# Performance work log

Measured on AMD Instinct MI355X. Metric: run time of the kernel, lower is better.

## Reference

```python
import jax, jax.numpy as jnp
import numpy as np

B, C, H, W = 2, 64, 64, 64
C2 = C // 2
N = H * W


def conv1x1(x, w, b):
    # x: (B,Cin,H,W), w: (Cout,Cin), b: (Cout,)
    return jnp.einsum('bchw,oc->bohw', x, w) + b[None, :, None, None]


def setup_inputs() -> dict:
    key = jax.random.key(0)
    ks = jax.random.split(key, 20)
    s = 0.05
    d = {
        'x1': jax.random.normal(ks[0], (B, C, H, W), jnp.float32),
        'x2': jax.random.normal(ks[1], (B, C, H, W), jnp.float32),
        'wq1': jax.random.normal(ks[2], (C2, C), jnp.float32) * s,
        'bq1': jax.random.normal(ks[3], (C2,), jnp.float32) * s,
        'wk1': jax.random.normal(ks[4], (C2, C), jnp.float32) * s,
        'bk1': jax.random.normal(ks[5], (C2,), jnp.float32) * s,
        'wv1': jax.random.normal(ks[6], (C2, C), jnp.float32) * s,
        'bv1': jax.random.normal(ks[7], (C2,), jnp.float32) * s,
        'wc1': jax.random.normal(ks[8], (C, C2), jnp.float32) * s,
        'bc1': jax.random.normal(ks[9], (C,), jnp.float32) * s,
        'wq2': jax.random.normal(ks[10], (C2, C), jnp.float32) * s,
        'bq2': jax.random.normal(ks[11], (C2,), jnp.float32) * s,
        'wk2': jax.random.normal(ks[12], (C2, C), jnp.float32) * s,
        'bk2': jax.random.normal(ks[13], (C2,), jnp.float32) * s,
        'wv2': jax.random.normal(ks[14], (C2, C), jnp.float32) * s,
        'bv2': jax.random.normal(ks[15], (C2,), jnp.float32) * s,
        'wc2': jax.random.normal(ks[16], (C, C2), jnp.float32) * s,
        'bc2': jax.random.normal(ks[17], (C,), jnp.float32) * s,
        'gamma1': jax.random.normal(ks[18], (1,), jnp.float32) * 0.5,
        'gamma2': jax.random.normal(ks[19], (1,), jnp.float32) * 0.5,
    }
    return d


def reference(x1, x2, wq1, bq1, wk1, bk1, wv1, bv1, wc1, bc1,
              wq2, bq2, wk2, bk2, wv2, bv2, wc2, bc2, gamma1, gamma2):
    b, c, h, w = x1.shape
    n = h * w
    # branch-1 projections (boundary semantics)
    q1 = jnp.max(conv1x1(x1, wq1, bq1), axis=1).reshape(b, n)          # (B,N) channel-max
    k1 = jnp.max(conv1x1(x1, wk1, bk1).reshape(b, -1, n), axis=1)      # (B,N)
    v1 = conv1x1(x1, wv1, bv1).reshape(b, -1, n)                        # (B,C/2,N)
    # branch-2 projections (field semantics)
    q2 = jnp.mean(conv1x1(x2, wq2, bq2), axis=1).reshape(b, n)         # (B,N) channel-mean
    k2 = jnp.mean(conv1x1(x2, wk2, bk2).reshape(b, -1, n), axis=1)     # (B,N)
    v2 = conv1x1(x2, wv2, bv2).reshape(b, -1, n)                        # (B,C/2,N)
    # energy2 = q1 (B,N,1) @ k2 (B,1,N) outer product; inverted sigmoid gate
    att2 = 1.0 - jax.nn.sigmoid(q1[:, :, None] * k2[:, None, :])        # (B,N,N)
    out1 = jnp.einsum('bck,bmk->bcm', v1, att2).reshape(b, c // 2, h, w)
    out1 = conv1x1(out1, wc2, bc2)
    # energy1 = q2 outer k1; sigmoid gate
    att1 = jax.nn.sigmoid(q2[:, :, None] * k1[:, None, :])              # (B,N,N)
    out2 = jnp.einsum('bck,bmk->bcm', v2, att1).reshape(b, c // 2, h, w)
    out2 = conv1x1(out2, wc1, bc1)
    out1 = x1 + gamma1[0] * out1
    out2 = x2 + gamma2[0] * out2
    return (out1, out2)
```

## Files before the change

### kernel.cpp

```cpp
#include <hip/hip_runtime.h>

#define NN 4096
#define CC 64
#define C2 32
#define BB 2

#define NSEG   4
#define M_BLK  64
#define KBLK   64
#define KB_ITERS (NN / NSEG / KBLK)

#define WS_Q1 0
#define WS_K1 8192
#define WS_Q2 16384
#define WS_K2 24576
#define WS_V1 32768
#define WS_V2 163840
#define WS_P  294912

typedef __attribute__((address_space(1))) const unsigned int GUI;
typedef __attribute__((address_space(3))) unsigned int LUI;
typedef __attribute__((ext_vector_type(8))) short bf16x8;
typedef __attribute__((ext_vector_type(4))) float f32x4;

__device__ __forceinline__ void glds16(const void* g, void* l) {
    __builtin_amdgcn_global_load_lds((GUI*)g, (LUI*)l, 16, 0, 0);
}

__device__ __forceinline__ unsigned short bf16_rne(float f) {
    union { float f; unsigned u; } x; x.f = f;
    unsigned u = x.u + 0x7fff + ((x.u >> 16) & 1);
    return (unsigned short)(u >> 16);
}
__device__ __forceinline__ unsigned pack2(float a, float b) {
    return (unsigned)bf16_rne(a) | ((unsigned)bf16_rne(b) << 16);
}
__device__ __forceinline__ float sigm_e2(float x) {
    return __builtin_amdgcn_rcpf(1.0f + __builtin_amdgcn_exp2f(x));
}

__global__ __launch_bounds__(256) void proj_kernel(
    const float* __restrict__ x1, const float* __restrict__ x2,
    const float* __restrict__ wq1, const float* __restrict__ bq1,
    const float* __restrict__ wk1, const float* __restrict__ bk1,
    const float* __restrict__ wv1, const float* __restrict__ bv1,
    const float* __restrict__ wq2, const float* __restrict__ bq2,
    const float* __restrict__ wk2, const float* __restrict__ bk2,
    const float* __restrict__ wv2, const float* __restrict__ bv2,
    float* __restrict__ ws)
{
    const int ln = threadIdx.x & 63;
    const int og = threadIdx.x >> 6;
    const int n  = blockIdx.x * 64 + ln;
    const int p  = blockIdx.y;
    const int b  = blockIdx.z;

    const float* x; const float* w; const float* bias;
    int mode; float* dstf; unsigned short* dstv;
    switch (p) {
      case 0: x = x1; w = wq1; bias = bq1; mode = 0; dstf = ws + WS_Q1; dstv = 0; break;
      case 1: x = x1; w = wk1; bias = bk1; mode = 0; dstf = ws + WS_K1; dstv = 0; break;
      case 2: x = x1; w = wv1; bias = bv1; mode = 2; dstf = 0; dstv = (unsigned short*)(ws + WS_V1); break;
      case 3: x = x2; w = wq2; bias = bq2; mode = 1; dstf = ws + WS_Q2; dstv = 0; break;
      case 4: x = x2; w = wk2; bias = bk2; mode = 1; dstf = ws + WS_K2; dstv = 0; break;
      default:x = x2; w = wv2; bias = bv2; mode = 2; dstf = 0; dstv = (unsigned short*)(ws + WS_V2); break;
    }

    __shared__ float red[4][C2][64];

    float acc[C2];
    #pragma unroll
    for (int o = 0; o < C2; ++o) acc[o] = 0.0f;

    const float* xb = x + ((size_t)b * CC + og * 16) * NN + n;
    #pragma unroll
    for (int ci = 0; ci < 16; ++ci) {
        const float xv = xb[(size_t)ci * NN];
        #pragma unroll
        for (int o = 0; o < C2; ++o)
            acc[o] += w[o * CC + og * 16 + ci] * xv;
    }
    #pragma unroll
    for (int o = 0; o < C2; ++o) red[og][o][ln] = acc[o];
    __syncthreads();

    float f[8];
    #pragma unroll
    for (int j = 0; j < 8; ++j) {
        const int o = og * 8 + j;
        f[j] = red[0][o][ln] + red[1][o][ln] + red[2][o][ln] + red[3][o][ln]
             + bias[o];
    }

    if (mode == 2) {
        #pragma unroll
        for (int j = 0; j < 8; ++j)
            dstv[((size_t)b * C2 + og * 8 + j) * NN + n] = bf16_rne(f[j]);
    } else {
        float r;
        if (mode == 0) {
            r = f[0];
            #pragma unroll
            for (int j = 1; j < 8; ++j) r = fmaxf(r, f[j]);
        } else {
            r = 0.0f;
            #pragma unroll
            for (int j = 0; j < 8; ++j) r += f[j];
        }
        __syncthreads();
        red[og][0][ln] = r;
        __syncthreads();
        if (og == 0) {
            const float a0 = red[0][0][ln], a1 = red[1][0][ln];
            const float a2 = red[2][0][ln], a3 = red[3][0][ln];
            const float rr = (mode == 0)
                ? fmaxf(fmaxf(a0, a1), fmaxf(a2, a3))
                : (a0 + a1 + a2 + a3) * (1.0f / C2);
            dstf[(size_t)b * NN + n] = rr;
        }
    }
}

__global__ __launch_bounds__(256) void attn_mfma(
    const float* __restrict__ q1, const float* __restrict__ k1,
    const float* __restrict__ q2, const float* __restrict__ k2,
    const unsigned short* __restrict__ v1, const unsigned short* __restrict__ v2,
    float* __restrict__ pout)
{
    __shared__ unsigned short vtile[C2 * KBLK];
    __shared__ unsigned short stile[M_BLK * KBLK];

    const int tid = threadIdx.x;
    const int wv  = tid >> 6;
    const int ln  = tid & 63;

    const int seg    = blockIdx.y;
    const int z      = blockIdx.z;
    const int branch = z & 1;
    const int b      = z >> 1;
    const int m0     = blockIdx.x * M_BLK;
    const int kstart = seg * (NN / NSEG);

    const float* q; const float* kv; const unsigned short* vbf; float sl2e;
    if (branch == 0) { q = q1; kv = k2; vbf = v1; sl2e =  1.44269504089f; }
    else             { q = q2; kv = k1; vbf = v2; sl2e = -1.44269504089f; }

    const float qs = q[(size_t)b * NN + m0 + ln] * sl2e;

    f32x4 acc[4];
    #pragma unroll
    for (int mt = 0; mt < 4; ++mt) acc[mt] = (f32x4){0.f, 0.f, 0.f, 0.f};

    const int vc = tid >> 3;
    const int vs = tid & 7;
    const unsigned short* vsrc0 = vbf + (size_t)(b * C2 + vc) * NN
                                + ((vs ^ (vc & 7)) << 3);

    for (int kb = 0; kb < KB_ITERS; ++kb) {
        const int k0 = kstart + kb * KBLK;

        glds16(vsrc0 + k0, (char*)vtile + tid * 16);

        const float* kvp = kv + (size_t)b * NN + k0 + (wv << 4);
        const float4 ka = *(const float4*)(kvp);
        const float4 kb4 = *(const float4*)(kvp + 4);
        const float4 kc = *(const float4*)(kvp + 8);
        const float4 kd = *(const float4*)(kvp + 12);

        float s[16];
        s[0]  = sigm_e2(qs * ka.x);  s[1]  = sigm_e2(qs * ka.y);
        s[2]  = sigm_e2(qs * ka.z);  s[3]  = sigm_e2(qs * ka.w);
        s[4]  = sigm_e2(qs * kb4.x); s[5]  = sigm_e2(qs * kb4.y);
        s[6]  = sigm_e2(qs * kb4.z); s[7]  = sigm_e2(qs * kb4.w);
        s[8]  = sigm_e2(qs * kc.x);  s[9]  = sigm_e2(qs * kc.y);
        s[10] = sigm_e2(qs * kc.z);  s[11] = sigm_e2(qs * kc.w);
        s[12] = sigm_e2(qs * kd.x);  s[13] = sigm_e2(qs * kd.y);
        s[14] = sigm_e2(qs * kd.z);  s[15] = sigm_e2(qs * kd.w);

        uint4 w0, w1;
        w0.x = pack2(s[0],  s[1]);  w0.y = pack2(s[2],  s[3]);
        w0.z = pack2(s[4],  s[5]);  w0.w = pack2(s[6],  s[7]);
        w1.x = pack2(s[8],  s[9]);  w1.y = pack2(s[10], s[11]);
        w1.z = pack2(s[12], s[13]); w1.w = pack2(s[14], s[15]);

        char* srow = (char*)stile + ln * 128;
        *(uint4*)(srow + ((((wv << 1) | 0) ^ (ln & 7)) << 4)) = w0;
        *(uint4*)(srow + ((((wv << 1) | 1) ^ (ln & 7)) << 4)) = w1;

        asm volatile("s_waitcnt vmcnt(0)" ::: "memory");
        __syncthreads();

        const int ct  = wv & 1;
        const int ks  = wv >> 1;
        const int col = (ks << 2) + (ln >> 4);
        const int ac  = ct * 16 + (ln & 15);
        const bf16x8 af = *(const bf16x8*)((const char*)vtile
                          + ac * 128 + ((col ^ (ac & 7)) << 4));
        #pragma unroll
        for (int mt = 0; mt < 4; ++mt) {
            const int bm = mt * 16 + (ln & 15);
            const bf16x8 bfr = *(const bf16x8*)((const char*)stile
                               + bm * 128 + ((col ^ (bm & 7)) << 4));
            acc[mt] = __builtin_amdgcn_mfma_f32_16x16x32_bf16(af, bfr, acc[mt], 0, 0, 0);
        }
        __syncthreads();
    }

    float* red = (float*)stile;
    if (wv >= 2) {
        #pragma unroll
        for (int mt = 0; mt < 4; ++mt)
            *(f32x4*)&red[((wv - 2) * 4 + mt) * 256 + ln * 4] = acc[mt];
    }
    __syncthreads();
    if (wv < 2) {
        const size_t obase = (((size_t)(branch * NSEG + seg) * BB + b) * C2) * NN;
        #pragma unroll
        for (int mt = 0; mt < 4; ++mt) {
            const f32x4 o = *(const f32x4*)&red[(wv * 4 + mt) * 256 + ln * 4];
            acc[mt].x += o.x; acc[mt].y += o.y; acc[mt].z += o.z; acc[mt].w += o.w;
            #pragma unroll
            for (int j = 0; j < 4; ++j) {
                const int c = wv * 16 + (ln >> 4) * 4 + j;
                const int m = m0 + mt * 16 + (ln & 15);
                pout[obase + (size_t)c * NN + m] = acc[mt][j];
            }
        }
    }
}

__global__ __launch_bounds__(256) void reduce_kernel(float* __restrict__ p, int nseg)
{
    const int t      = blockIdx.x * 256 + threadIdx.x;
    const int m4     = t & 1023;
    const int c      = (t >> 10) & 31;
    const int b      = (t >> 15) & 1;
    const int branch = t >> 16;

    const size_t segstride = (size_t)BB * C2 * NN;
    const float* base = p + ((size_t)branch * nseg * BB + b) * C2 * NN
                          + (size_t)c * NN + m4 * 4;

    float4 acc = *(const float4*)base;
    for (int s = 1; s < nseg; ++s) {
        const float4 v = *(const float4*)(base + s * segstride);
        acc.x += v.x; acc.y += v.y; acc.z += v.z; acc.w += v.w;
    }
    *(float4*)(p + ((size_t)branch * nseg * BB + b) * C2 * NN
                 + (size_t)c * NN + m4 * 4) = acc;
}

__global__ __launch_bounds__(256) void conv_kernel(
    const float* __restrict__ x1, const float* __restrict__ x2,
    const float* __restrict__ wc1, const float* __restrict__ bc1,
    const float* __restrict__ wc2, const float* __restrict__ bc2,
    const float* __restrict__ g1,  const float* __restrict__ g2,
    const float* __restrict__ p,   float* __restrict__ out, int nseg)
{
    const int m      = blockIdx.x * 256 + threadIdx.x;
    const int co0    = blockIdx.y * 8;
    const int b      = blockIdx.z >> 1;
    const int branch = blockIdx.z & 1;

    const float* w; const float* bias; const float* x; float gamma; float* o;
    if (branch == 0) { w = wc2; bias = bc2; x = x1; gamma = g1[0]; o = out; }
    else             { w = wc1; bias = bc1; x = x2; gamma = g2[0]; o = out + (size_t)BB * CC * NN; }

    const float* sbase = p + ((size_t)branch * nseg * BB + b) * C2 * NN + m;
    float s[C2];
    #pragma unroll
    for (int c = 0; c < C2; ++c) s[c] = sbase[(size_t)c * NN];

    #pragma unroll
    for (int co = co0; co < co0 + 8; ++co) {
        float a = bias[co];
        #pragma unroll
        for (int c = 0; c < C2; ++c)
            a += w[co * C2 + c] * s[c];
        const size_t idx = ((size_t)b * CC + co) * NN + m;
        o[idx] = x[idx] + gamma * a;
    }
}

extern "C" void kernel_launch(void* const* d_in, const int* in_sizes, int n_in,
                              void* d_out, int out_size, void* d_ws, size_t ws_size,
                              hipStream_t stream)
{
    const float* x1  = (const float*)d_in[0];
    const float* x2  = (const float*)d_in[1];
    const float* wq1 = (const float*)d_in[2];
    const float* bq1 = (const float*)d_in[3];
    const float* wk1 = (const float*)d_in[4];
    const float* bk1 = (const float*)d_in[5];
    const float* wv1 = (const float*)d_in[6];
    const float* bv1 = (const float*)d_in[7];
    const float* wc1 = (const float*)d_in[8];
    const float* bc1 = (const float*)d_in[9];
    const float* wq2 = (const float*)d_in[10];
    const float* bq2 = (const float*)d_in[11];
    const float* wk2 = (const float*)d_in[12];
    const float* bk2 = (const float*)d_in[13];
    const float* wv2 = (const float*)d_in[14];
    const float* bv2 = (const float*)d_in[15];
    const float* wc2 = (const float*)d_in[16];
    const float* bc2 = (const float*)d_in[17];
    const float* g1  = (const float*)d_in[18];
    const float* g2  = (const float*)d_in[19];

    float* ws  = (float*)d_ws;
    float* out = (float*)d_out;

    proj_kernel<<<dim3(NN / 64, 6, BB), 256, 0, stream>>>(
        x1, x2, wq1, bq1, wk1, bk1, wv1, bv1,
        wq2, bq2, wk2, bk2, wv2, bv2, ws);

    const float* q1 = ws + WS_Q1; const float* k1 = ws + WS_K1;
    const float* q2 = ws + WS_Q2; const float* k2 = ws + WS_K2;
    const unsigned short* v1 = (const unsigned short*)(ws + WS_V1);
    const unsigned short* v2 = (const unsigned short*)(ws + WS_V2);
    float* pp = ws + WS_P;

    attn_mfma<<<dim3(NN / M_BLK, NSEG, BB * 2), 256, 0, stream>>>(
        q1, k1, q2, k2, v1, v2, pp);

    reduce_kernel<<<dim3(512), 256, 0, stream>>>(pp, NSEG);

    conv_kernel<<<dim3(NN / 256, 8, BB * 2), 256, 0, stream>>>(
        x1, x2, wc1, bc1, wc2, bc2, g1, g2, pp, out, NSEG);
}
```

Before: 56.70 us.

## Double-buffer attention LDS tiles and fold segment reduction into conv kernel

The attention kernel now uses two LDS buffers for the V and sigmoid tiles. It prefetches the next V tile and computes the next sigmoid tile while MFMAs run on the current one, which cuts one barrier per iteration. The separate reduce kernel is removed, and the conv kernel sums the four segment partials itself. This saves a launch and a write/read pass, but each conv block re-reads the partials (8 output-channel groups each load all segments), and the doubled LDS may lower occupancy.

```diff
diff --git a/kernel.cpp b/kernel.cpp
--- a/kernel.cpp
+++ b/kernel.cpp
@@ -127,8 +127,8 @@
     const unsigned short* __restrict__ v1, const unsigned short* __restrict__ v2,
     float* __restrict__ pout)
 {
-    __shared__ unsigned short vtile[C2 * KBLK];
-    __shared__ unsigned short stile[M_BLK * KBLK];
+    __shared__ unsigned short vtile[2][C2 * KBLK];
+    __shared__ unsigned short stile[2][M_BLK * KBLK];
 
     const int tid = threadIdx.x;
     const int wv  = tid >> 6;
@@ -146,6 +146,7 @@
     else             { q = q2; kv = k1; vbf = v2; sl2e = -1.44269504089f; }
 
     const float qs = q[(size_t)b * NN + m0 + ln] * sl2e;
+    const float* kvb = kv + (size_t)b * NN;
 
     f32x4 acc[4];
     #pragma unroll
@@ -156,16 +157,12 @@
     const unsigned short* vsrc0 = vbf + (size_t)(b * C2 + vc) * NN
                                 + ((vs ^ (vc & 7)) << 3);
 
-    for (int kb = 0; kb < KB_ITERS; ++kb) {
-        const int k0 = kstart + kb * KBLK;
-
-        glds16(vsrc0 + k0, (char*)vtile + tid * 16);
-
-        const float* kvp = kv + (size_t)b * NN + k0 + (wv << 4);
-        const float4 ka = *(const float4*)(kvp);
+    auto computeS = [&](int buf, int k0) {
+        const float* kvp = kvb + k0 + (wv << 4);
+        const float4 ka  = *(const float4*)(kvp);
         const float4 kb4 = *(const float4*)(kvp + 4);
-        const float4 kc = *(const float4*)(kvp + 8);
-        const float4 kd = *(const float4*)(kvp + 12);
+        const float4 kc  = *(const float4*)(kvp + 8);
+        const float4 kd  = *(const float4*)(kvp + 12);
 
         float s[16];
         s[0]  = sigm_e2(qs * ka.x);  s[1]  = sigm_e2(qs * ka.y);
@@ -183,26 +180,43 @@
         w1.x = pack2(s[8],  s[9]);  w1.y = pack2(s[10], s[11]);
         w1.z = pack2(s[12], s[13]); w1.w = pack2(s[14], s[15]);
 
-        char* srow = (char*)stile + ln * 128;
+        char* srow = (char*)stile[buf] + ln * 128;
         *(uint4*)(srow + ((((wv << 1) | 0) ^ (ln & 7)) << 4)) = w0;
         *(uint4*)(srow + ((((wv << 1) | 1) ^ (ln & 7)) << 4)) = w1;
-
-        asm volatile("s_waitcnt vmcnt(0)" ::: "memory");
-        __syncthreads();
-
-        const int ct  = wv & 1;
-        const int ks  = wv >> 1;
-        const int col = (ks << 2) + (ln >> 4);
-        const int ac  = ct * 16 + (ln & 15);
-        const bf16x8 af = *(const bf16x8*)((const char*)vtile
+    };
+
+    glds16(vsrc0 + kstart, (char*)vtile[0] + tid * 16);
+    computeS(0, kstart);
+    asm volatile("s_waitcnt vmcnt(0)" ::: "memory");
+    __syncthreads();
+
+    const int ct = wv & 1;
+    const int ks = wv >> 1;
+    const int col = (ks << 2) + (ln >> 4);
+    const int ac  = ct * 16 + (ln & 15);
+
+    #pragma unroll 2
+    for (int kb = 0; kb < KB_ITERS; ++kb) {
+        const int cur = kb & 1;
+
+        if (kb + 1 < KB_ITERS)
+            glds16(vsrc0 + kstart + (kb + 1) * KBLK,
+                   (char*)vtile[cur ^ 1] + tid * 16);
+
+        const bf16x8 af = *(const bf16x8*)((const char*)vtile[cur]
                           + ac * 128 + ((col ^ (ac & 7)) << 4));
         #pragma unroll
         for (int mt = 0; mt < 4; ++mt) {
             const int bm = mt * 16 + (ln & 15);
-            const bf16x8 bfr = *(const bf16x8*)((const char*)stile
+            const bf16x8 bfr = *(const bf16x8*)((const char*)stile[cur]
                                + bm * 128 + ((col ^ (bm & 7)) << 4));
             acc[mt] = __builtin_amdgcn_mfma_f32_16x16x32_bf16(af, bfr, acc[mt], 0, 0, 0);
         }
+
+        if (kb + 1 < KB_ITERS)
+            computeS(cur ^ 1, kstart + (kb + 1) * KBLK);
+
+        asm volatile("s_waitcnt vmcnt(0)" ::: "memory");
         __syncthreads();
     }
 
@@ -229,33 +243,12 @@
     }
 }
 
-__global__ __launch_bounds__(256) void reduce_kernel(float* __restrict__ p, int nseg)
-{
-    const int t      = blockIdx.x * 256 + threadIdx.x;
-    const int m4     = t & 1023;
-    const int c      = (t >> 10) & 31;
-    const int b      = (t >> 15) & 1;
-    const int branch = t >> 16;
-
-    const size_t segstride = (size_t)BB * C2 * NN;
-    const float* base = p + ((size_t)branch * nseg * BB + b) * C2 * NN
-                          + (size_t)c * NN + m4 * 4;
-
-    float4 acc = *(const float4*)base;
-    for (int s = 1; s < nseg; ++s) {
-        const float4 v = *(const float4*)(base + s * segstride);
-        acc.x += v.x; acc.y += v.y; acc.z += v.z; acc.w += v.w;
-    }
-    *(float4*)(p + ((size_t)branch * nseg * BB + b) * C2 * NN
-                 + (size_t)c * NN + m4 * 4) = acc;
-}
-
 __global__ __launch_bounds__(256) void conv_kernel(
     const float* __restrict__ x1, const float* __restrict__ x2,
     const float* __restrict__ wc1, const float* __restrict__ bc1,
     const float* __restrict__ wc2, const float* __restrict__ bc2,
     const float* __restrict__ g1,  const float* __restrict__ g2,
-    const float* __restrict__ p,   float* __restrict__ out, int nseg)
+    const float* __restrict__ p,   float* __restrict__ out)
 {
     const int m      = blockIdx.x * 256 + threadIdx.x;
     const int co0    = blockIdx.y * 8;
@@ -266,10 +259,16 @@
     if (branch == 0) { w = wc2; bias = bc2; x = x1; gamma = g1[0]; o = out; }
     else             { w = wc1; bias = bc1; x = x2; gamma = g2[0]; o = out + (size_t)BB * CC * NN; }
 
-    const float* sbase = p + ((size_t)branch * nseg * BB + b) * C2 * NN + m;
     float s[C2];
     #pragma unroll
-    for (int c = 0; c < C2; ++c) s[c] = sbase[(size_t)c * NN];
+    for (int c = 0; c < C2; ++c) s[c] = 0.0f;
+    #pragma unroll
+    for (int seg = 0; seg < NSEG; ++seg) {
+        const float* sb = p + (((size_t)(branch * NSEG + seg) * BB + b) * C2) * NN + m;
+        #pragma unroll
+        for (int c = 0; c < C2; ++c)
+            s[c] += sb[(size_t)c * NN];
+    }
 
     #pragma unroll
     for (int co = co0; co < co0 + 8; ++co) {
@@ -323,8 +322,6 @@
     attn_mfma<<<dim3(NN / M_BLK, NSEG, BB * 2), 256, 0, stream>>>(
         q1, k1, q2, k2, v1, v2, pp);
 
-    reduce_kernel<<<dim3(512), 256, 0, stream>>>(pp, NSEG);
-
     conv_kernel<<<dim3(NN / 256, 8, BB * 2), 256, 0, stream>>>(
-        x1, x2, wc1, bc1, wc2, bc2, g1, g2, pp, out, NSEG);
-}
+        x1, x2, wc1, bc1, wc2, bc2, g1, g2, pp, out);
+}
```

Measured after the change: 75.45 us. 1.33x slower.
